# Performance work log

Measured on AMD Instinct MI355X. Metric: run time of the kernel, lower is better.

The kernel has to match this reference:

```python
import jax, jax.numpy as jnp
import numpy as np
import math

IN_FEATURES = 3072
PADDED = 4096  # next power of two
ACT_BITS = 8
LN_EPS = 1e-6


def hadamard_transform(x):
    """Normalized fast Walsh-Hadamard transform along last dim (power of 2)."""
    n = x.shape[-1]
    m = n.bit_length() - 1  # log2(n)
    shape = x.shape
    y = x.reshape(shape[:-1] + (2,) * m)
    for ax in range(len(shape) - 1, len(shape) - 1 + m):
        a = jnp.take(y, 0, axis=ax)
        b = jnp.take(y, 1, axis=ax)
        y = jnp.stack([a + b, a - b], axis=ax)
    return y.reshape(shape) / jnp.sqrt(jnp.asarray(n, x.dtype))


def activation_quant(x, bits=ACT_BITS):
    """Per-token absmax int-b quant with STE (BitNet style)."""
    qb = 2 ** (bits - 1) - 1  # 127
    scale = qb / jnp.clip(jnp.max(jnp.abs(x), axis=-1, keepdims=True), 1e-5)
    q = jnp.clip(jnp.round(x * scale), -qb - 1, qb) / scale
    return x + jax.lax.stop_gradient(q - x)


def weight_quant(w):
    """Ternary absmean weight quant with STE (as in training path)."""
    scale = jnp.clip(jnp.mean(jnp.abs(w)), 1e-5)
    q = jnp.clip(jnp.round(w / scale), -1.0, 1.0) * scale
    return w + jax.lax.stop_gradient(q - w)


def layer_norm(x, gamma, beta, eps=LN_EPS):
    mu = jnp.mean(x, axis=-1, keepdims=True)
    var = jnp.mean(jnp.square(x - mu), axis=-1, keepdims=True)
    return (x - mu) * jax.lax.rsqrt(var + eps) * gamma + beta


def setup_inputs() -> dict:
    key = jax.random.key(0)
    k1, k2 = jax.random.split(key)
    x = jax.random.normal(k1, (4, 2048, IN_FEATURES), dtype=jnp.float32)
    ln_gamma = jnp.ones((IN_FEATURES,), dtype=jnp.float32)
    ln_beta = jnp.zeros((IN_FEATURES,), dtype=jnp.float32)
    weight = jax.random.normal(k2, (4096, PADDED), dtype=jnp.float32) * 0.02
    return {"x": x, "ln_gamma": ln_gamma, "ln_beta": ln_beta, "weight": weight}


def reference(x, ln_gamma, ln_beta, weight):
    x_norm = layer_norm(x, ln_gamma, ln_beta)
    pad = PADDED - IN_FEATURES
    x_pad = jnp.pad(x_norm, ((0, 0), (0, 0), (0, pad)))
    x_had = hadamard_transform(x_pad)
    x_q = activation_quant(x_had)
    w_q = weight_quant(weight)
    # F.linear: x @ W^T
    out = jnp.einsum('bsd,od->bso', x_q, w_q)
    return out
```

## Files before the change

### kernel.cpp

```cpp
#include <hip/hip_runtime.h>
#include <stdint.h>

#define TOKENS 8192
#define IN_F   3072
#define PAD_F  4096
#define N_OUT  4096
#define K_DIM  4096

using i32x4 = __attribute__((ext_vector_type(4))) int;

#define Q_OFF    0
#define WQ_OFF   33554432
#define AINV_OFF 50331648
#define PART_OFF 50364416
#define WSC_OFF  50380800

__device__ __forceinline__ void gload_lds16(const void* g, void* l) {
    __builtin_amdgcn_global_load_lds(
        (__attribute__((address_space(1))) void*)(void*)g,
        (__attribute__((address_space(3))) void*)l,
        16, 0, 0);
}

__global__ __launch_bounds__(256) void k_wabs(const float* __restrict__ w,
                                              float* __restrict__ partial) {
    int tid = threadIdx.x;
    const float4* w4 = (const float4*)(w + (size_t)blockIdx.x * 4096);
    float s = 0.f;
#pragma unroll
    for (int i = 0; i < 4; ++i) {
        float4 v = w4[tid + i * 256];
        s += fabsf(v.x) + fabsf(v.y) + fabsf(v.z) + fabsf(v.w);
    }
#pragma unroll
    for (int o = 32; o > 0; o >>= 1) s += __shfl_xor(s, o);
    __shared__ float rb[4];
    if ((tid & 63) == 0) rb[tid >> 6] = s;
    __syncthreads();
    if (tid == 0) partial[blockIdx.x] = rb[0] + rb[1] + rb[2] + rb[3];
}

__global__ __launch_bounds__(256) void k_wscale(const float* __restrict__ partial,
                                                float* __restrict__ wsp) {
    int tid = threadIdx.x;
    float s = 0.f;
#pragma unroll
    for (int i = 0; i < 16; ++i) s += partial[tid + i * 256];
#pragma unroll
    for (int o = 32; o > 0; o >>= 1) s += __shfl_xor(s, o);
    __shared__ float rb[4];
    if ((tid & 63) == 0) rb[tid >> 6] = s;
    __syncthreads();
    if (tid == 0)
        wsp[0] = fmaxf((rb[0] + rb[1] + rb[2] + rb[3]) * (1.0f / 16777216.0f), 1e-5f);
}

__global__ __launch_bounds__(256) void k_wquant(const float* __restrict__ w,
                                                const float* __restrict__ wsp,
                                                unsigned int* __restrict__ wq) {
    int idx = blockIdx.x * 256 + threadIdx.x;
    float ws = wsp[0];
    float4 v = ((const float4*)w)[idx];
    int a = (int)rintf(v.x / ws); a = max(-1, min(1, a));
    int b = (int)rintf(v.y / ws); b = max(-1, min(1, b));
    int c = (int)rintf(v.z / ws); c = max(-1, min(1, c));
    int d = (int)rintf(v.w / ws); d = max(-1, min(1, d));
    unsigned int p = (unsigned)(a & 255) | ((unsigned)(b & 255) << 8) |
                     ((unsigned)(c & 255) << 16) | ((unsigned)(d & 255) << 24);
    wq[idx] = p;
}

__global__ __launch_bounds__(256) void k_lnfwht(const float* __restrict__ x,
                                                const float* __restrict__ gamma,
                                                const float* __restrict__ beta,
                                                unsigned int* __restrict__ q,
                                                float* __restrict__ ainv) {
    __shared__ float s[PAD_F];
    __shared__ float rb[8];
    int tid = threadIdx.x;
    int t = blockIdx.x;
    const float* xr = x + (size_t)t * IN_F;

    float v[12];
    float sum = 0.f;
#pragma unroll
    for (int i = 0; i < 12; ++i) { v[i] = xr[tid + i * 256]; sum += v[i]; }
#pragma unroll
    for (int o = 32; o > 0; o >>= 1) sum += __shfl_xor(sum, o);
    if ((tid & 63) == 0) rb[tid >> 6] = sum;
    __syncthreads();
    float mu = (rb[0] + rb[1] + rb[2] + rb[3]) * (1.0f / 3072.0f);

    float s2 = 0.f;
#pragma unroll
    for (int i = 0; i < 12; ++i) { float d = v[i] - mu; s2 += d * d; }
#pragma unroll
    for (int o = 32; o > 0; o >>= 1) s2 += __shfl_xor(s2, o);
    if ((tid & 63) == 0) rb[4 + (tid >> 6)] = s2;
    __syncthreads();
    float var = (rb[4] + rb[5] + rb[6] + rb[7]) * (1.0f / 3072.0f);
    float rstd = 1.0f / sqrtf(var + 1e-6f);

#pragma unroll
    for (int i = 0; i < 12; ++i) {
        int idx = tid + i * 256;
        s[idx] = (v[i] - mu) * rstd * gamma[idx] + beta[idx];
    }
#pragma unroll
    for (int i = 0; i < 4; ++i) s[IN_F + tid + i * 256] = 0.f;
    __syncthreads();

    for (int h = 1; h < PAD_F; h <<= 1) {
#pragma unroll
        for (int jj = 0; jj < 8; ++jj) {
            int j = tid + jj * 256;
            int i0 = ((j & ~(h - 1)) << 1) | (j & (h - 1));
            float a = s[i0], b = s[i0 + h];
            s[i0] = a + b;
            s[i0 + h] = a - b;
        }
        __syncthreads();
    }

    float mx = 0.f;
#pragma unroll
    for (int i = 0; i < 16; ++i) mx = fmaxf(mx, fabsf(s[tid + i * 256]));
#pragma unroll
    for (int o = 32; o > 0; o >>= 1) mx = fmaxf(mx, __shfl_xor(mx, o));
    if ((tid & 63) == 0) rb[tid >> 6] = mx;
    __syncthreads();
    float amraw = fmaxf(fmaxf(rb[0], rb[1]), fmaxf(rb[2], rb[3]));
    float amax = fmaxf(amraw * (1.0f / 64.0f), 1e-5f);
    float scale = 127.0f / amax;
    if (tid == 0) ainv[t] = amax * (1.0f / 127.0f);

    unsigned int* qr = q + (size_t)t * (PAD_F / 4);
#pragma unroll
    for (int i = 0; i < 4; ++i) {
        int g = tid + i * 256;
        unsigned int p = 0;
#pragma unroll
        for (int e = 0; e < 4; ++e) {
            float xh = s[4 * g + e] * (1.0f / 64.0f);
            int qi = (int)rintf(xh * scale);
            qi = max(-128, min(127, qi));
            p |= (unsigned)(qi & 255) << (8 * e);
        }
        qr[g] = p;
    }
}

#define NT 32

__global__ __launch_bounds__(512, 2) void k_gemm(const signed char* __restrict__ Aq,
                                                 const signed char* __restrict__ Wq,
                                                 const float* __restrict__ ainv,
                                                 const float* __restrict__ wsp,
                                                 float* __restrict__ out) {
    __shared__ signed char sA[2][256 * 128];
    __shared__ signed char sB[2][256 * 128];

    int tid = threadIdx.x;
    int lane = tid & 63, wid = tid >> 6;

    int bid = blockIdx.x;
    int swz = (bid & 7) * 64 + (bid >> 3);
    int bmb = swz & 31;
    int bnb = swz >> 5;
    size_t bm0 = (size_t)bmb * 256, bn0 = (size_t)bnb * 256;

    int wm = wid >> 2, wn = wid & 3;
    int l8 = lane >> 3, l7 = lane & 7;
    int lrow = lane & 15, hi = lane >> 4;

    const signed char* gA = Aq + (bm0 + (size_t)(wid * 32 + l8)) * K_DIM + (size_t)((l7 ^ l8) * 16);
    const signed char* gB = Wq + (bn0 + (size_t)(wid * 32 + l8)) * K_DIM + (size_t)((l7 ^ l8) * 16);

    i32x4 acc[8][4];
#pragma unroll
    for (int m = 0; m < 8; ++m)
#pragma unroll
        for (int n = 0; n < 4; ++n) acc[m][n] = (i32x4){0, 0, 0, 0};

    int abase = (wm * 128 + lrow) * 8;
    int bbase = (wn * 64 + lrow) * 8;

    auto STAGE = [&](int b, int k0) {
#pragma unroll
        for (int i = 0; i < 4; ++i) {
            gload_lds16(gA + (size_t)k0 + (size_t)i * 8 * K_DIM, &sA[b][(wid * 32 + i * 8) * 128]);
            gload_lds16(gB + (size_t)k0 + (size_t)i * 8 * K_DIM, &sB[b][(wid * 32 + i * 8) * 128]);
        }
    };

    auto COMPUTE = [&](int b) {
        const i32x4* va = (const i32x4*)&sA[b][0];
        const i32x4* vb = (const i32x4*)&sB[b][0];
#pragma unroll
        for (int ks = 0; ks < 2; ++ks) {
            int kx = (ks * 4 + hi) ^ l7;
            i32x4 af[8], bf[4];
#pragma unroll
            for (int m = 0; m < 8; ++m) af[m] = va[abase + m * 128 + kx];
#pragma unroll
            for (int n = 0; n < 4; ++n) bf[n] = vb[bbase + n * 128 + kx];
            __builtin_amdgcn_s_setprio(1);
#pragma unroll
            for (int m = 0; m < 8; ++m)
#pragma unroll
                for (int n = 0; n < 4; ++n)
                    acc[m][n] = __builtin_amdgcn_mfma_i32_16x16x64_i8(af[m], bf[n], acc[m][n], 0, 0, 0);
            __builtin_amdgcn_s_setprio(0);
        }
    };

    STAGE(0, 0);
    __syncthreads();

#pragma unroll 1
    for (int t = 0; t < NT - 1; ++t) {
        STAGE((t + 1) & 1, (t + 1) * 128);
        COMPUTE(t & 1);
        __syncthreads();
    }
    COMPUTE((NT - 1) & 1);

    float wsc = wsp[0];
#pragma unroll
    for (int m = 0; m < 8; ++m) {
        size_t row0 = bm0 + wm * 128 + m * 16 + hi * 4;
#pragma unroll
        for (int r = 0; r < 4; ++r) {
            size_t row = row0 + r;
            float sa = wsc * ainv[row];
#pragma unroll
            for (int n = 0; n < 4; ++n) {
                size_t col = bn0 + wn * 64 + n * 16 + lrow;
                out[row * N_OUT + col] = (float)acc[m][n][r] * sa;
            }
        }
    }
}

extern "C" void kernel_launch(void* const* d_in, const int* in_sizes, int n_in,
                              void* d_out, int out_size, void* d_ws, size_t ws_size,
                              hipStream_t stream) {
    const float* x     = (const float*)d_in[0];
    const float* gamma = (const float*)d_in[1];
    const float* beta  = (const float*)d_in[2];
    const float* w     = (const float*)d_in[3];
    float* out = (float*)d_out;
    char* ws = (char*)d_ws;

    signed char* q   = (signed char*)(ws + Q_OFF);
    signed char* wq  = (signed char*)(ws + WQ_OFF);
    float* ainv      = (float*)(ws + AINV_OFF);
    float* partial   = (float*)(ws + PART_OFF);
    float* wsp       = (float*)(ws + WSC_OFF);

    k_wabs<<<dim3(4096), dim3(256), 0, stream>>>(w, partial);
    k_wscale<<<dim3(1), dim3(256), 0, stream>>>(partial, wsp);
    k_wquant<<<dim3(16384), dim3(256), 0, stream>>>(w, wsp, (unsigned int*)wq);
    k_lnfwht<<<dim3(TOKENS), dim3(256), 0, stream>>>(x, gamma, beta, (unsigned int*)q, ainv);
    k_gemm<<<dim3(512), dim3(512), 0, stream>>>(q, wq, ainv, wsp, out);
}
```

Before: 251.1 us.

## Register/shuffle FWHT and 4-stage BK=64 GEMM pipeline with XCD-aware tiling

The LN+FWHT kernel now runs the Hadamard butterflies in registers: in-thread stages first, then wave shuffles, then two LDS exchange rounds. This replaces twelve barrier-separated shared-memory passes, and the quantized bytes are stored directly. The int8 GEMM moves from a double-buffered K=128 tile to a four-stage ring of K=64 tiles, with explicit vmcnt waits and s_barrier so global-to-LDS loads overlap compute three tiles ahead. Block-to-tile mapping is changed to group M tiles per XCD for cache locality. In exchange the kernel carries more LDS buffers, more barriers per K step, and fragile hand-written waitcnt counts.

```diff
diff --git a/kernel.cpp b/kernel.cpp
--- a/kernel.cpp
+++ b/kernel.cpp
@@ -73,18 +73,20 @@
 __global__ __launch_bounds__(256) void k_lnfwht(const float* __restrict__ x,
                                                 const float* __restrict__ gamma,
                                                 const float* __restrict__ beta,
-                                                unsigned int* __restrict__ q,
+                                                signed char* __restrict__ q,
                                                 float* __restrict__ ainv) {
     __shared__ float s[PAD_F];
     __shared__ float rb[8];
     int tid = threadIdx.x;
+    int lane = tid & 63;
     int t = blockIdx.x;
     const float* xr = x + (size_t)t * IN_F;
 
-    float v[12];
+    float v[16];
     float sum = 0.f;
 #pragma unroll
     for (int i = 0; i < 12; ++i) { v[i] = xr[tid + i * 256]; sum += v[i]; }
+    v[12] = v[13] = v[14] = v[15] = 0.f;
 #pragma unroll
     for (int o = 32; o > 0; o >>= 1) sum += __shfl_xor(sum, o);
     if ((tid & 63) == 0) rb[tid >> 6] = sum;
@@ -102,31 +104,47 @@
     float rstd = 1.0f / sqrtf(var + 1e-6f);
 
 #pragma unroll
-    for (int i = 0; i < 12; ++i) {
-        int idx = tid + i * 256;
-        s[idx] = (v[i] - mu) * rstd * gamma[idx] + beta[idx];
-    }
-#pragma unroll
-    for (int i = 0; i < 4; ++i) s[IN_F + tid + i * 256] = 0.f;
-    __syncthreads();
-
-    for (int h = 1; h < PAD_F; h <<= 1) {
-#pragma unroll
-        for (int jj = 0; jj < 8; ++jj) {
-            int j = tid + jj * 256;
-            int i0 = ((j & ~(h - 1)) << 1) | (j & (h - 1));
-            float a = s[i0], b = s[i0 + h];
-            s[i0] = a + b;
-            s[i0 + h] = a - b;
-        }
+    for (int i = 0; i < 12; ++i)
+        v[i] = (v[i] - mu) * rstd * gamma[tid + i * 256] + beta[tid + i * 256];
+
+#pragma unroll
+    for (int b = 1; b < 16; b <<= 1) {
+#pragma unroll
+        for (int i = 0; i < 16; ++i) {
+            if (!(i & b)) {
+                float a0 = v[i], b0 = v[i | b];
+                v[i] = a0 + b0;
+                v[i | b] = a0 - b0;
+            }
+        }
+    }
+#pragma unroll
+    for (int m = 1; m <= 32; m <<= 1) {
+#pragma unroll
+        for (int i = 0; i < 16; ++i) {
+            float p = __shfl_xor(v[i], m);
+            v[i] = (lane & m) ? (p - v[i]) : (v[i] + p);
+        }
+    }
+#pragma unroll
+    for (int m = 64; m <= 128; m <<= 1) {
         __syncthreads();
+#pragma unroll
+        for (int i = 0; i < 16; ++i) s[tid + i * 256] = v[i];
+        __syncthreads();
+#pragma unroll
+        for (int i = 0; i < 16; ++i) {
+            float p = s[(tid ^ m) + i * 256];
+            v[i] = (tid & m) ? (p - v[i]) : (v[i] + p);
+        }
     }
 
     float mx = 0.f;
 #pragma unroll
-    for (int i = 0; i < 16; ++i) mx = fmaxf(mx, fabsf(s[tid + i * 256]));
+    for (int i = 0; i < 16; ++i) mx = fmaxf(mx, fabsf(v[i]));
 #pragma unroll
     for (int o = 32; o > 0; o >>= 1) mx = fmaxf(mx, __shfl_xor(mx, o));
+    __syncthreads();
     if ((tid & 63) == 0) rb[tid >> 6] = mx;
     __syncthreads();
     float amraw = fmaxf(fmaxf(rb[0], rb[1]), fmaxf(rb[2], rb[3]));
@@ -134,47 +152,42 @@
     float scale = 127.0f / amax;
     if (tid == 0) ainv[t] = amax * (1.0f / 127.0f);
 
-    unsigned int* qr = q + (size_t)t * (PAD_F / 4);
-#pragma unroll
-    for (int i = 0; i < 4; ++i) {
-        int g = tid + i * 256;
-        unsigned int p = 0;
-#pragma unroll
-        for (int e = 0; e < 4; ++e) {
-            float xh = s[4 * g + e] * (1.0f / 64.0f);
-            int qi = (int)rintf(xh * scale);
-            qi = max(-128, min(127, qi));
-            p |= (unsigned)(qi & 255) << (8 * e);
-        }
-        qr[g] = p;
-    }
-}
-
-#define NT 32
+    signed char* qr = q + (size_t)t * PAD_F;
+#pragma unroll
+    for (int i = 0; i < 16; ++i) {
+        int qi = (int)rintf(v[i] * (1.0f / 64.0f) * scale);
+        qi = max(-128, min(127, qi));
+        qr[tid + i * 256] = (signed char)qi;
+    }
+}
+
+#define BK 64
+#define NT (K_DIM / BK)
 
 __global__ __launch_bounds__(512, 2) void k_gemm(const signed char* __restrict__ Aq,
                                                  const signed char* __restrict__ Wq,
                                                  const float* __restrict__ ainv,
                                                  const float* __restrict__ wsp,
                                                  float* __restrict__ out) {
-    __shared__ signed char sA[2][256 * 128];
-    __shared__ signed char sB[2][256 * 128];
+    __shared__ signed char sA[4][256 * BK];
+    __shared__ signed char sB[4][256 * BK];
 
     int tid = threadIdx.x;
     int lane = tid & 63, wid = tid >> 6;
 
     int bid = blockIdx.x;
-    int swz = (bid & 7) * 64 + (bid >> 3);
-    int bmb = swz & 31;
-    int bnb = swz >> 5;
+    int xcd = bid & 7, li = bid >> 3;
+    int bmb = xcd * 4 + (li & 3);
+    int bnb = li >> 2;
     size_t bm0 = (size_t)bmb * 256, bn0 = (size_t)bnb * 256;
 
     int wm = wid >> 2, wn = wid & 3;
-    int l8 = lane >> 3, l7 = lane & 7;
     int lrow = lane & 15, hi = lane >> 4;
 
-    const signed char* gA = Aq + (bm0 + (size_t)(wid * 32 + l8)) * K_DIM + (size_t)((l7 ^ l8) * 16);
-    const signed char* gB = Wq + (bn0 + (size_t)(wid * 32 + l8)) * K_DIM + (size_t)((l7 ^ l8) * 16);
+    int srow = lane >> 2;
+    int schunk = (lane & 3) ^ ((lane >> 3) & 3);
+    const signed char* gA = Aq + (bm0 + (size_t)(wid * 32 + srow)) * K_DIM + schunk * 16;
+    const signed char* gB = Wq + (bn0 + (size_t)(wid * 32 + srow)) * K_DIM + schunk * 16;
 
     i32x4 acc[8][4];
 #pragma unroll
@@ -182,48 +195,61 @@
 #pragma unroll
         for (int n = 0; n < 4; ++n) acc[m][n] = (i32x4){0, 0, 0, 0};
 
-    int abase = (wm * 128 + lrow) * 8;
-    int bbase = (wn * 64 + lrow) * 8;
-
-    auto STAGE = [&](int b, int k0) {
-#pragma unroll
-        for (int i = 0; i < 4; ++i) {
-            gload_lds16(gA + (size_t)k0 + (size_t)i * 8 * K_DIM, &sA[b][(wid * 32 + i * 8) * 128]);
-            gload_lds16(gB + (size_t)k0 + (size_t)i * 8 * K_DIM, &sB[b][(wid * 32 + i * 8) * 128]);
-        }
+    int kx = hi ^ ((lane >> 1) & 3);
+    int abase = (wm * 128 + lrow) * 4 + kx;
+    int bbase = (wn * 64 + lrow) * 4 + kx;
+
+    auto STAGE = [&](int b, int t) {
+        size_t k0 = (size_t)t * BK;
+        gload_lds16(gA + k0, &sA[b][(wid * 32) * BK]);
+        gload_lds16(gA + k0 + (size_t)16 * K_DIM, &sA[b][(wid * 32 + 16) * BK]);
+        gload_lds16(gB + k0, &sB[b][(wid * 32) * BK]);
+        gload_lds16(gB + k0 + (size_t)16 * K_DIM, &sB[b][(wid * 32 + 16) * BK]);
     };
 
     auto COMPUTE = [&](int b) {
         const i32x4* va = (const i32x4*)&sA[b][0];
         const i32x4* vb = (const i32x4*)&sB[b][0];
-#pragma unroll
-        for (int ks = 0; ks < 2; ++ks) {
-            int kx = (ks * 4 + hi) ^ l7;
-            i32x4 af[8], bf[4];
-#pragma unroll
-            for (int m = 0; m < 8; ++m) af[m] = va[abase + m * 128 + kx];
-#pragma unroll
-            for (int n = 0; n < 4; ++n) bf[n] = vb[bbase + n * 128 + kx];
-            __builtin_amdgcn_s_setprio(1);
-#pragma unroll
-            for (int m = 0; m < 8; ++m)
-#pragma unroll
-                for (int n = 0; n < 4; ++n)
-                    acc[m][n] = __builtin_amdgcn_mfma_i32_16x16x64_i8(af[m], bf[n], acc[m][n], 0, 0, 0);
-            __builtin_amdgcn_s_setprio(0);
-        }
+        i32x4 af[8], bf[4];
+#pragma unroll
+        for (int m = 0; m < 8; ++m) af[m] = va[abase + m * 64];
+#pragma unroll
+        for (int n = 0; n < 4; ++n) bf[n] = vb[bbase + n * 64];
+        __builtin_amdgcn_s_setprio(1);
+#pragma unroll
+        for (int m = 0; m < 8; ++m)
+#pragma unroll
+            for (int n = 0; n < 4; ++n)
+                acc[m][n] = __builtin_amdgcn_mfma_i32_16x16x64_i8(af[m], bf[n], acc[m][n], 0, 0, 0);
+        __builtin_amdgcn_s_setprio(0);
     };
 
     STAGE(0, 0);
-    __syncthreads();
+    STAGE(1, 1);
+    STAGE(2, 2);
 
 #pragma unroll 1
-    for (int t = 0; t < NT - 1; ++t) {
-        STAGE((t + 1) & 1, (t + 1) * 128);
-        COMPUTE(t & 1);
-        __syncthreads();
-    }
-    COMPUTE((NT - 1) & 1);
+    for (int t = 0; t < NT - 3; ++t) {
+        STAGE((t + 3) & 3, t + 3);
+        asm volatile("s_waitcnt vmcnt(12)" ::: "memory");
+        __builtin_amdgcn_s_barrier();
+        __builtin_amdgcn_sched_barrier(0);
+        COMPUTE(t & 3);
+        __builtin_amdgcn_sched_barrier(0);
+        __builtin_amdgcn_s_barrier();
+    }
+    asm volatile("s_waitcnt vmcnt(8)" ::: "memory");
+    __builtin_amdgcn_s_barrier();
+    __builtin_amdgcn_sched_barrier(0);
+    COMPUTE((NT - 3) & 3);
+    asm volatile("s_waitcnt vmcnt(4)" ::: "memory");
+    __builtin_amdgcn_s_barrier();
+    __builtin_amdgcn_sched_barrier(0);
+    COMPUTE((NT - 2) & 3);
+    asm volatile("s_waitcnt vmcnt(0)" ::: "memory");
+    __builtin_amdgcn_s_barrier();
+    __builtin_amdgcn_sched_barrier(0);
+    COMPUTE((NT - 1) & 3);
 
     float wsc = wsp[0];
 #pragma unroll
@@ -261,6 +287,6 @@
     k_wabs<<<dim3(4096), dim3(256), 0, stream>>>(w, partial);
     k_wscale<<<dim3(1), dim3(256), 0, stream>>>(partial, wsp);
     k_wquant<<<dim3(16384), dim3(256), 0, stream>>>(w, wsp, (unsigned int*)wq);
-    k_lnfwht<<<dim3(TOKENS), dim3(256), 0, stream>>>(x, gamma, beta, (unsigned int*)q, ainv);
+    k_lnfwht<<<dim3(TOKENS), dim3(256), 0, stream>>>(x, gamma, beta, q, ainv);
     k_gemm<<<dim3(512), dim3(512), 0, stream>>>(q, wq, ainv, wsp, out);
 }
```

After: 244.8 us. 1.03x faster.
